# Kernel optimization log

Measured on AMD Instinct MI355X. Metric: run time of the kernel, lower is better.

Reference implementation:

```python
import jax, jax.numpy as jnp
import numpy as np

KERNEL_SIZE = 5
BANDWIDTH = 1.0
N_KERNELS = KERNEL_SIZE * KERNEL_SIZE - 1  # 24, center tap excluded
PAD = KERNEL_SIZE // 2


def _offsets():
    # one-hot kernel index for slot i skips the center position
    offs = []
    for i in range(N_KERNELS):
        idx = i if i < N_KERNELS // 2 else i + 1
        offs.append((idx // KERNEL_SIZE, idx % KERNEL_SIZE))
    return offs


def setup_inputs() -> dict:
    key = jax.random.key(0)
    X = jax.random.normal(key, (4, 3, 512, 512), dtype=jnp.float32)
    return {"X": X}


def reference(X) -> jnp.ndarray:
    B, C, H, W = X.shape
    # zero padding matches Conv2d(padding=k//2, bias=False) with one-hot weights
    Xp = jnp.pad(X, ((0, 0), (0, 0), (PAD, PAD), (PAD, PAD)))
    # the grouped one-hot conv is just a neighbor-shift gather:
    # Xj[:, :, i, h, w] = Xp[:, :, h + r_i, w + c_i]
    Xj = jnp.stack([Xp[:, :, r:r + H, c:c + W] for (r, c) in _offsets()], axis=2)
    Xi = X[:, :, None, :, :]  # [B, C, 1, H, W]
    inv = 1.0 / (2.0 * BANDWIDTH * BANDWIDTH)
    K = jnp.exp(-((Xj - Xi) ** 2) * inv)  # [B, C, n_kernels, H, W]
    return K
```

## Files before the change

### kernel.cpp

```cpp
#include <hip/hip_runtime.h>


#define HH 512
#define WW 512
#define NPLANES 12
#define NK 24

typedef float f32x4 __attribute__((ext_vector_type(4)));

extern "C" __device__ float __builtin_amdgcn_exp2f(float);

__global__ __launch_bounds__(256) void gauss_mask_kernel(
    const float* __restrict__ X, float* __restrict__ out)
{
    const int tid = blockIdx.x * blockDim.x + threadIdx.x;
    const int p   = tid >> 16;
    const int rem = tid & 65535;
    const int h   = rem >> 7;
    const int w0  = (rem & 127) << 2;

    const float* Xp = X + (size_t)p * (HH * WW);

    const f32x4 xi4 = *reinterpret_cast<const f32x4*>(Xp + (size_t)h * WW + w0);
    float xiv[4] = {xi4.x, xi4.y, xi4.z, xi4.w};

    float rows[5][8];
    #pragma unroll
    for (int dr = 0; dr < 5; ++dr) {
        const int hh = h + dr - 2;
        const bool rok = (hh >= 0) && (hh < HH);
        const float* rptr = Xp + (size_t)hh * WW;
        #pragma unroll
        for (int j = 0; j < 8; ++j) {
            const int ww = w0 + j - 2;
            rows[dr][j] = (rok && ww >= 0 && ww < WW) ? rptr[ww] : 0.0f;
        }
    }

    const float c = -0.5f * 1.44269504088896340736f;

    float* outp = out + (size_t)p * NK * HH * WW + (size_t)h * WW + w0;

    #pragma unroll
    for (int k = 0; k < NK; ++k) {
        const int idx = (k < 12) ? k : k + 1;
        const int dr = idx / 5;
        const int dc = idx % 5;
        f32x4 v;
        #pragma unroll
        for (int i = 0; i < 4; ++i) {
            const float d = rows[dr][dc + i] - xiv[i];
            v[i] = __builtin_amdgcn_exp2f(d * d * c);
        }
        __builtin_nontemporal_store(v, reinterpret_cast<f32x4*>(outp + (size_t)k * (HH * WW)));
    }
}

extern "C" void kernel_launch(void* const* d_in, const int* in_sizes, int n_in,
                              void* d_out, int out_size, void* d_ws, size_t ws_size,
                              hipStream_t stream) {
    const float* X = (const float*)d_in[0];
    float* out = (float*)d_out;

    const int total = NPLANES * HH * (WW / 4);
    const int block = 256;
    const int grid = total / block;
    gauss_mask_kernel<<<grid, block, 0, stream>>>(X, out);
}
```

Baseline: 55.68 us.

## Compute 4x4 output tile per thread with vectorized halo window loads

Each thread now covers a 4x4 pixel tile instead of a 1x4 strip. It loads an 8x8 input window with aligned float4 loads, replacing the old per-element scalar halo loads. This cuts redundant input reads and address math, and the grid shrinks by a factor of four. The kernel is dominated by output writes, so the gain may be small, and fewer threads with more registers each could reduce how well memory latency is hidden.

```diff
diff --git a/kernel.cpp b/kernel.cpp
--- a/kernel.cpp
+++ b/kernel.cpp
@@ -5,6 +5,7 @@
 #define WW 512
 #define NPLANES 12
 #define NK 24
+#define HW (HH * WW)
 
 typedef float f32x4 __attribute__((ext_vector_type(4)));
 
@@ -14,45 +15,61 @@
     const float* __restrict__ X, float* __restrict__ out)
 {
     const int tid = blockIdx.x * blockDim.x + threadIdx.x;
-    const int p   = tid >> 16;
-    const int rem = tid & 65535;
-    const int h   = rem >> 7;
+    const int p   = tid >> 14;
+    const int rem = tid & 16383;
+    const int h0  = (rem >> 7) << 2;
     const int w0  = (rem & 127) << 2;
 
-    const float* Xp = X + (size_t)p * (HH * WW);
+    const float* Xp = X + (size_t)p * HW;
 
-    const f32x4 xi4 = *reinterpret_cast<const f32x4*>(Xp + (size_t)h * WW + w0);
-    float xiv[4] = {xi4.x, xi4.y, xi4.z, xi4.w};
+    const bool wl = (w0 > 0);
+    const bool wr = (w0 < WW - 4);
+    const int  aL = wl ? w0 - 4 : 0;
+    const int  aR = wr ? w0 + 4 : WW - 4;
 
-    float rows[5][8];
+    float win[8][8];
     #pragma unroll
-    for (int dr = 0; dr < 5; ++dr) {
-        const int hh = h + dr - 2;
-        const bool rok = (hh >= 0) && (hh < HH);
-        const float* rptr = Xp + (size_t)hh * WW;
-        #pragma unroll
-        for (int j = 0; j < 8; ++j) {
-            const int ww = w0 + j - 2;
-            rows[dr][j] = (rok && ww >= 0 && ww < WW) ? rptr[ww] : 0.0f;
+    for (int r = 0; r < 8; ++r) {
+        const int hh = h0 + r - 2;
+        if (hh >= 0 && hh < HH) {
+            const float* rp = Xp + (size_t)hh * WW;
+            const f32x4 qL = *reinterpret_cast<const f32x4*>(rp + aL);
+            const f32x4 qC = *reinterpret_cast<const f32x4*>(rp + w0);
+            const f32x4 qR = *reinterpret_cast<const f32x4*>(rp + aR);
+            win[r][0] = wl ? qL[2] : 0.0f;
+            win[r][1] = wl ? qL[3] : 0.0f;
+            win[r][2] = qC[0];
+            win[r][3] = qC[1];
+            win[r][4] = qC[2];
+            win[r][5] = qC[3];
+            win[r][6] = wr ? qR[0] : 0.0f;
+            win[r][7] = wr ? qR[1] : 0.0f;
+        } else {
+            #pragma unroll
+            for (int j = 0; j < 8; ++j) win[r][j] = 0.0f;
         }
     }
 
     const float c = -0.5f * 1.44269504088896340736f;
 
-    float* outp = out + (size_t)p * NK * HH * WW + (size_t)h * WW + w0;
+    float* outp = out + (size_t)p * NK * HW + (size_t)h0 * WW + w0;
 
     #pragma unroll
     for (int k = 0; k < NK; ++k) {
         const int idx = (k < 12) ? k : k + 1;
         const int dr = idx / 5;
         const int dc = idx % 5;
-        f32x4 v;
+        float* kp = outp + (size_t)k * HW;
         #pragma unroll
-        for (int i = 0; i < 4; ++i) {
-            const float d = rows[dr][dc + i] - xiv[i];
-            v[i] = __builtin_amdgcn_exp2f(d * d * c);
+        for (int hr = 0; hr < 4; ++hr) {
+            f32x4 v;
+            #pragma unroll
+            for (int i = 0; i < 4; ++i) {
+                const float d = win[hr + dr][dc + i] - win[hr + 2][2 + i];
+                v[i] = __builtin_amdgcn_exp2f(d * d * c);
+            }
+            __builtin_nontemporal_store(v, reinterpret_cast<f32x4*>(kp + (size_t)hr * WW));
         }
-        __builtin_nontemporal_store(v, reinterpret_cast<f32x4*>(outp + (size_t)k * (HH * WW)));
     }
 }
 
@@ -62,7 +79,7 @@
     const float* X = (const float*)d_in[0];
     float* out = (float*)d_out;
 
-    const int total = NPLANES * HH * (WW / 4);
+    const int total = NPLANES * (HH / 4) * (WW / 4);
     const int block = 256;
     const int grid = total / block;
     gauss_mask_kernel<<<grid, block, 0, stream>>>(X, out);
```

Result: slower. 63.68 us (+14.4%).

## Split work across output kernel slots via 2D grid with per-slot templated gather

Applied to the files above, without the earlier changes.

Each thread now computes a single output slot k (chosen by blockIdx.y) for four pixels, where before it computed all 24 slots. Neighbor values come from aligned float4 loads with lane shuffling, replacing scalar loads. Block size is raised to 512 and the grid grows 24x. The aim is more parallelism and a contiguous write stream per block, at the cost of re-reading the input 24 times, which should mostly hit in cache.

```diff
diff --git a/kernel.cpp b/kernel.cpp
--- a/kernel.cpp
+++ b/kernel.cpp
@@ -5,54 +5,109 @@
 #define WW 512
 #define NPLANES 12
 #define NK 24
+#define HW (HH * WW)
 
 typedef float f32x4 __attribute__((ext_vector_type(4)));
 
 extern "C" __device__ float __builtin_amdgcn_exp2f(float);
 
-__global__ __launch_bounds__(256) void gauss_mask_kernel(
+template <int DR, int DC>
+__device__ __forceinline__ void do_case(const float* __restrict__ Xp,
+                                        float* __restrict__ kp,
+                                        int h, int w0)
+{
+    const float c = -0.5f * 1.44269504088896340736f;
+    const float* ctr_row = Xp + (size_t)h * WW;
+    const f32x4 xc = *reinterpret_cast<const f32x4*>(ctr_row + w0);
+
+    const int hh = h + DR - 2;
+    f32x4 nb;
+    if (hh >= 0 && hh < HH) {
+        const float* nr = Xp + (size_t)hh * WW;
+        if constexpr (DC == 2) {
+            nb = *reinterpret_cast<const f32x4*>(nr + w0);
+        } else if constexpr (DC < 2) {
+            const f32x4 qC = *reinterpret_cast<const f32x4*>(nr + w0);
+            const f32x4 qA = *reinterpret_cast<const f32x4*>(nr + (w0 > 0 ? w0 - 4 : 0));
+            constexpr int off = DC - 2;
+            #pragma unroll
+            for (int i = 0; i < 4; ++i) {
+                if constexpr (off + 100) {}
+                float v;
+                if (off + i < 0) {
+                    v = (w0 > 0) ? qA[4 + off + i] : 0.0f;
+                } else {
+                    v = qC[off + i];
+                }
+                nb[i] = v;
+            }
+        } else {
+            const f32x4 qC = *reinterpret_cast<const f32x4*>(nr + w0);
+            const f32x4 qB = *reinterpret_cast<const f32x4*>(nr + (w0 < WW - 4 ? w0 + 4 : WW - 4));
+            constexpr int off = DC - 2;
+            #pragma unroll
+            for (int i = 0; i < 4; ++i) {
+                float v;
+                if (off + i > 3) {
+                    v = (w0 < WW - 4) ? qB[off + i - 4] : 0.0f;
+                } else {
+                    v = qC[off + i];
+                }
+                nb[i] = v;
+            }
+        }
+    } else {
+        #pragma unroll
+        for (int i = 0; i < 4; ++i) nb[i] = 0.0f;
+    }
+
+    f32x4 v;
+    #pragma unroll
+    for (int i = 0; i < 4; ++i) {
+        const float d = nb[i] - xc[i];
+        v[i] = __builtin_amdgcn_exp2f(d * d * c);
+    }
+    __builtin_nontemporal_store(v, reinterpret_cast<f32x4*>(kp + (size_t)h * WW + w0));
+}
+
+__global__ __launch_bounds__(512) void gauss_mask_kernel(
     const float* __restrict__ X, float* __restrict__ out)
 {
-    const int tid = blockIdx.x * blockDim.x + threadIdx.x;
-    const int p   = tid >> 16;
-    const int rem = tid & 65535;
+    const int idx = blockIdx.x * 512 + threadIdx.x;
+    const int p   = idx >> 16;
+    const int rem = idx & 65535;
     const int h   = rem >> 7;
     const int w0  = (rem & 127) << 2;
+    const int k   = blockIdx.y;
 
-    const float* Xp = X + (size_t)p * (HH * WW);
+    const float* Xp = X + (size_t)p * HW;
+    float* kp = out + ((size_t)p * NK + k) * HW;
 
-    const f32x4 xi4 = *reinterpret_cast<const f32x4*>(Xp + (size_t)h * WW + w0);
-    float xiv[4] = {xi4.x, xi4.y, xi4.z, xi4.w};
-
-    float rows[5][8];
-    #pragma unroll
-    for (int dr = 0; dr < 5; ++dr) {
-        const int hh = h + dr - 2;
-        const bool rok = (hh >= 0) && (hh < HH);
-        const float* rptr = Xp + (size_t)hh * WW;
-        #pragma unroll
-        for (int j = 0; j < 8; ++j) {
-            const int ww = w0 + j - 2;
-            rows[dr][j] = (rok && ww >= 0 && ww < WW) ? rptr[ww] : 0.0f;
-        }
-    }
-
-    const float c = -0.5f * 1.44269504088896340736f;
-
-    float* outp = out + (size_t)p * NK * HH * WW + (size_t)h * WW + w0;
-
-    #pragma unroll
-    for (int k = 0; k < NK; ++k) {
-        const int idx = (k < 12) ? k : k + 1;
-        const int dr = idx / 5;
-        const int dc = idx % 5;
-        f32x4 v;
-        #pragma unroll
-        for (int i = 0; i < 4; ++i) {
-            const float d = rows[dr][dc + i] - xiv[i];
-            v[i] = __builtin_amdgcn_exp2f(d * d * c);
-        }
-        __builtin_nontemporal_store(v, reinterpret_cast<f32x4*>(outp + (size_t)k * (HH * WW)));
+    switch (k) {
+        case  0: do_case<0, 0>(Xp, kp, h, w0); break;
+        case  1: do_case<0, 1>(Xp, kp, h, w0); break;
+        case  2: do_case<0, 2>(Xp, kp, h, w0); break;
+        case  3: do_case<0, 3>(Xp, kp, h, w0); break;
+        case  4: do_case<0, 4>(Xp, kp, h, w0); break;
+        case  5: do_case<1, 0>(Xp, kp, h, w0); break;
+        case  6: do_case<1, 1>(Xp, kp, h, w0); break;
+        case  7: do_case<1, 2>(Xp, kp, h, w0); break;
+        case  8: do_case<1, 3>(Xp, kp, h, w0); break;
+        case  9: do_case<1, 4>(Xp, kp, h, w0); break;
+        case 10: do_case<2, 0>(Xp, kp, h, w0); break;
+        case 11: do_case<2, 1>(Xp, kp, h, w0); break;
+        case 12: do_case<2, 3>(Xp, kp, h, w0); break;
+        case 13: do_case<2, 4>(Xp, kp, h, w0); break;
+        case 14: do_case<3, 0>(Xp, kp, h, w0); break;
+        case 15: do_case<3, 1>(Xp, kp, h, w0); break;
+        case 16: do_case<3, 2>(Xp, kp, h, w0); break;
+        case 17: do_case<3, 3>(Xp, kp, h, w0); break;
+        case 18: do_case<3, 4>(Xp, kp, h, w0); break;
+        case 19: do_case<4, 0>(Xp, kp, h, w0); break;
+        case 20: do_case<4, 1>(Xp, kp, h, w0); break;
+        case 21: do_case<4, 2>(Xp, kp, h, w0); break;
+        case 22: do_case<4, 3>(Xp, kp, h, w0); break;
+        case 23: do_case<4, 4>(Xp, kp, h, w0); break;
     }
 }
 
@@ -62,8 +117,6 @@
     const float* X = (const float*)d_in[0];
     float* out = (float*)d_out;
 
-    const int total = NPLANES * HH * (WW / 4);
-    const int block = 256;
-    const int grid = total / block;
-    gauss_mask_kernel<<<grid, block, 0, stream>>>(X, out);
+    dim3 grid(1536, NK);
+    gauss_mask_kernel<<<grid, 512, 0, stream>>>(X, out);
 }
```

Result: faster. 53.84 us (-3.3%).

## Split work by neighbor row across grid.y and use vector row loads

Applied to the files above, without the earlier changes.

Each thread now handles a single neighbor row offset, chosen by blockIdx.y, and writes only the 4-5 output channels for that row instead of all 24. Neighbor values are read with three aligned 16-byte vector loads, with edge masking done on register lanes, in place of 40 scalar guarded loads. Block size rises to 512, giving five times more threads with lower register pressure. In exchange, the center row is reloaded by every row-slice and the X reads are repeated about five times, though these should mostly hit cache.

```diff
diff --git a/kernel.cpp b/kernel.cpp
--- a/kernel.cpp
+++ b/kernel.cpp
@@ -3,56 +3,84 @@
 
 #define HH 512
 #define WW 512
-#define NPLANES 12
 #define NK 24
+#define HW (HH * WW)
 
 typedef float f32x4 __attribute__((ext_vector_type(4)));
 
 extern "C" __device__ float __builtin_amdgcn_exp2f(float);
 
-__global__ __launch_bounds__(256) void gauss_mask_kernel(
+template <int DR>
+__device__ __forceinline__ void body(const float* __restrict__ Xp,
+                                     float* __restrict__ outp,
+                                     int h, int w0)
+{
+    const float c = -0.5f * 1.44269504088896340736f;
+    const f32x4 xc = *reinterpret_cast<const f32x4*>(Xp + (size_t)h * WW + w0);
+
+    const int hh = h + DR - 2;
+    const bool wl = (w0 > 0);
+    const bool wr = (w0 < WW - 4);
+    const bool rok = (DR == 2) || (hh >= 0 && hh < HH);
+
+    f32x4 qA, qC, qB;
+    if (rok) {
+        const float* nr = Xp + (size_t)hh * WW;
+        qC = (DR == 2) ? xc : *reinterpret_cast<const f32x4*>(nr + w0);
+        qA = *reinterpret_cast<const f32x4*>(nr + (wl ? w0 - 4 : 0));
+        qB = *reinterpret_cast<const f32x4*>(nr + (wr ? w0 + 4 : WW - 4));
+    } else {
+        qA = (f32x4){0.f, 0.f, 0.f, 0.f};
+        qC = (f32x4){0.f, 0.f, 0.f, 0.f};
+        qB = (f32x4){0.f, 0.f, 0.f, 0.f};
+    }
+
+    const float A2 = wl ? qA[2] : 0.f;
+    const float A3 = wl ? qA[3] : 0.f;
+    const float B0 = wr ? qB[0] : 0.f;
+    const float B1 = wr ? qB[1] : 0.f;
+
+    const float nb[5][4] = {
+        {A2,    A3,    qC[0], qC[1]},
+        {A3,    qC[0], qC[1], qC[2]},
+        {qC[0], qC[1], qC[2], qC[3]},
+        {qC[1], qC[2], qC[3], B0   },
+        {qC[2], qC[3], B0,    B1   },
+    };
+
+    #pragma unroll
+    for (int dc = 0; dc < 5; ++dc) {
+        if (DR == 2 && dc == 2) continue;
+        const int idx   = DR * 5 + dc;
+        const int out_k = (idx < 12) ? idx : idx - 1;
+        f32x4 v;
+        #pragma unroll
+        for (int i = 0; i < 4; ++i) {
+            const float d = nb[dc][i] - xc[i];
+            v[i] = __builtin_amdgcn_exp2f(d * d * c);
+        }
+        __builtin_nontemporal_store(v, reinterpret_cast<f32x4*>(outp + (size_t)out_k * HW));
+    }
+}
+
+__global__ __launch_bounds__(512) void gauss_mask_kernel(
     const float* __restrict__ X, float* __restrict__ out)
 {
-    const int tid = blockIdx.x * blockDim.x + threadIdx.x;
-    const int p   = tid >> 16;
-    const int rem = tid & 65535;
+    const int idx = blockIdx.x * 512 + threadIdx.x;
+    const int p   = idx >> 16;
+    const int rem = idx & 65535;
     const int h   = rem >> 7;
     const int w0  = (rem & 127) << 2;
 
-    const float* Xp = X + (size_t)p * (HH * WW);
+    const float* Xp = X + (size_t)p * HW;
+    float* outp = out + (size_t)p * NK * HW + (size_t)h * WW + w0;
 
-    const f32x4 xi4 = *reinterpret_cast<const f32x4*>(Xp + (size_t)h * WW + w0);
-    float xiv[4] = {xi4.x, xi4.y, xi4.z, xi4.w};
-
-    float rows[5][8];
-    #pragma unroll
-    for (int dr = 0; dr < 5; ++dr) {
-        const int hh = h + dr - 2;
-        const bool rok = (hh >= 0) && (hh < HH);
-        const float* rptr = Xp + (size_t)hh * WW;
-        #pragma unroll
-        for (int j = 0; j < 8; ++j) {
-            const int ww = w0 + j - 2;
-            rows[dr][j] = (rok && ww >= 0 && ww < WW) ? rptr[ww] : 0.0f;
-        }
-    }
-
-    const float c = -0.5f * 1.44269504088896340736f;
-
-    float* outp = out + (size_t)p * NK * HH * WW + (size_t)h * WW + w0;
-
-    #pragma unroll
-    for (int k = 0; k < NK; ++k) {
-        const int idx = (k < 12) ? k : k + 1;
-        const int dr = idx / 5;
-        const int dc = idx % 5;
-        f32x4 v;
-        #pragma unroll
-        for (int i = 0; i < 4; ++i) {
-            const float d = rows[dr][dc + i] - xiv[i];
-            v[i] = __builtin_amdgcn_exp2f(d * d * c);
-        }
-        __builtin_nontemporal_store(v, reinterpret_cast<f32x4*>(outp + (size_t)k * (HH * WW)));
+    switch (blockIdx.y) {
+        case 0: body<0>(Xp, outp, h, w0); break;
+        case 1: body<1>(Xp, outp, h, w0); break;
+        case 2: body<2>(Xp, outp, h, w0); break;
+        case 3: body<3>(Xp, outp, h, w0); break;
+        case 4: body<4>(Xp, outp, h, w0); break;
     }
 }
 
@@ -62,8 +90,6 @@
     const float* X = (const float*)d_in[0];
     float* out = (float*)d_out;
 
-    const int total = NPLANES * HH * (WW / 4);
-    const int block = 256;
-    const int grid = total / block;
-    gauss_mask_kernel<<<grid, block, 0, stream>>>(X, out);
+    dim3 grid(1536, 5);
+    gauss_mask_kernel<<<grid, 512, 0, stream>>>(X, out);
 }
```

New measurement: 57.70 us. 3.6% more time.
